# Kernel tuning notes

Hardware: AMD Instinct MI355X
Metric: run time of the kernel (lower is better)

The kernel has to match this reference:

```python
import jax, jax.numpy as jnp
import numpy as np
from jax import lax

N, D, H, E = 8192, 1024, 4096, 8


def setup_inputs() -> dict:
    key = jax.random.key(0)
    ks = jax.random.split(key, 7)
    s = 0.02
    return {
        "x": jax.random.normal(ks[0], (N, D), dtype=jnp.float32),
        "Wr": jax.random.normal(ks[1], (E, D), dtype=jnp.float32) * s,
        "br": jnp.zeros((E,), dtype=jnp.float32),
        "Wup": jax.random.normal(ks[2], (E, H, D), dtype=jnp.float32) * s,
        "bup": jnp.zeros((E, H), dtype=jnp.float32),
        "Wdown": jax.random.normal(ks[3], (E, D, H), dtype=jnp.float32) * s,
        "bdown": jnp.zeros((E, D), dtype=jnp.float32),
    }


def reference(x, Wr, br, Wup, bup, Wdown, bdown):
    # Router: softmax over logits; only argmax is used (softmax is monotone,
    # argmax of softmax == argmax of logits).
    logits = x @ Wr.T + br            # [N, E]
    scores = jax.nn.softmax(logits, axis=-1)
    top1 = jnp.argmax(scores, axis=-1)  # [N] int

    out0 = jnp.zeros_like(x)

    def body(out, ew):
        i, Wu, bu, Wd, bd = ew
        h = jax.nn.silu(x @ Wu.T + bu)   # [N, H]
        y = h @ Wd.T + bd                # [N, D]
        out = jnp.where((top1 == i)[:, None], y, out)
        return out, None

    idx = jnp.arange(Wup.shape[0])
    out, _ = lax.scan(body, out0, (idx, Wup, bup, Wdown, bdown))
    return out
```

## Files before the change

kernel.cpp:

```cpp
#include <hip/hip_runtime.h>

#define NT 8192
#define DD 1024
#define HH 4096
#define EE 8

typedef __attribute__((ext_vector_type(8))) short short8;
typedef __attribute__((ext_vector_type(4))) float f32x4;

__device__ __forceinline__ unsigned short f2bf(float f) {
    unsigned int u = __float_as_uint(f);
    u += 0x7FFFu + ((u >> 16) & 1u);
    return (unsigned short)(u >> 16);
}

__device__ __forceinline__ void gload_lds16(const void* g, void* l) {
    __builtin_amdgcn_global_load_lds(
        (const __attribute__((address_space(1))) unsigned int*)g,
        (__attribute__((address_space(3))) unsigned int*)l, 16, 0, 0);
}

__global__ __launch_bounds__(256) void cvt_kernel(const float* __restrict__ src,
                                                  unsigned short* __restrict__ dst) {
    size_t i = ((size_t)blockIdx.x * 256 + threadIdx.x) * 4;
    float4 v = *(const float4*)(src + i);
    ushort4 o;
    o.x = f2bf(v.x); o.y = f2bf(v.y); o.z = f2bf(v.z); o.w = f2bf(v.w);
    *(ushort4*)(dst + i) = o;
}

__global__ __launch_bounds__(256) void router_kernel(const float* __restrict__ x,
                                                     const float* __restrict__ Wr,
                                                     const float* __restrict__ br,
                                                     int* __restrict__ counts,
                                                     int* __restrict__ tlist) {
    __shared__ float sW[EE * DD];
    const int t = threadIdx.x;
    for (int i = t; i < EE * DD / 4; i += 256)
        ((float4*)sW)[i] = ((const float4*)Wr)[i];
    __syncthreads();
    const int lane = t & 63;
    const int wv = t >> 6;
    const int token = blockIdx.x * 4 + wv;
    const float* xr = x + (size_t)token * DD;
    float acc[EE];
#pragma unroll
    for (int e = 0; e < EE; e++) acc[e] = 0.f;
    for (int k = lane; k < DD; k += 64) {
        float xv = xr[k];
#pragma unroll
        for (int e = 0; e < EE; e++) acc[e] += xv * sW[e * DD + k];
    }
#pragma unroll
    for (int off = 32; off > 0; off >>= 1) {
#pragma unroll
        for (int e = 0; e < EE; e++) acc[e] += __shfl_xor(acc[e], off);
    }
    if (lane == 0) {
        int best = 0;
        float bv = acc[0] + br[0];
#pragma unroll
        for (int e = 1; e < EE; e++) {
            float v = acc[e] + br[e];
            if (v > bv) { bv = v; best = e; }
        }
        int pos = atomicAdd(&counts[best], 1);
        tlist[best * NT + pos] = token;
    }
}

__global__ void offsets_kernel(const int* __restrict__ counts, int* __restrict__ offsets) {
    if (threadIdx.x == 0) {
        int s = 0;
        for (int e = 0; e < EE; e++) { offsets[e] = s; s += counts[e]; }
    }
}

__global__ __launch_bounds__(256) void up_gemm(const unsigned short* __restrict__ xb,
                                               const unsigned short* __restrict__ Wub,
                                               const float* __restrict__ bup,
                                               const int* __restrict__ counts,
                                               const int* __restrict__ tlist,
                                               const int* __restrict__ offsets,
                                               unsigned short* __restrict__ hbuf) {
    const int e = blockIdx.z;
    const int cnt = counts[e];
    const int m0 = blockIdx.y * 128;
    if (m0 >= cnt) return;
    const int n0 = blockIdx.x * 128;
    const int t = threadIdx.x;

    __shared__ unsigned short sA[128 * 32];
    __shared__ unsigned short sB[128 * 32];

    const int r0 = t >> 2;
    const int kc = t & 3;
    const int* tl = tlist + e * NT;
    const int c1 = cnt - 1;
    int ra = m0 + r0;      if (ra > c1) ra = c1;
    int rb = m0 + 64 + r0; if (rb > c1) rb = c1;
    const unsigned short* gA0 = xb + (size_t)tl[ra] * DD + kc * 8;
    const unsigned short* gA1 = xb + (size_t)tl[rb] * DD + kc * 8;
    const unsigned short* gB0 = Wub + ((size_t)e * HH + n0 + r0) * DD + kc * 8;
    const unsigned short* gB1 = Wub + ((size_t)e * HH + n0 + 64 + r0) * DD + kc * 8;
    unsigned short* lA0 = sA + t * 8;
    unsigned short* lA1 = sA + (t + 256) * 8;
    unsigned short* lB0 = sB + t * 8;
    unsigned short* lB1 = sB + (t + 256) * 8;

    const int lane = t & 63;
    const int wm = ((t >> 6) & 1) * 64;
    const int wn = (t >> 7) * 64;
    const int mrow = lane & 15;
    const int kq = lane >> 4;

    f32x4 acc[4][4];
#pragma unroll
    for (int i = 0; i < 4; i++)
#pragma unroll
        for (int j = 0; j < 4; j++)
            acc[i][j] = (f32x4){0.f, 0.f, 0.f, 0.f};

    for (int kt = 0; kt < DD; kt += 32) {
        __syncthreads();
        gload_lds16(gA0 + kt, lA0);
        gload_lds16(gA1 + kt, lA1);
        gload_lds16(gB0 + kt, lB0);
        gload_lds16(gB1 + kt, lB1);
        __syncthreads();
        short8 a[4], b[4];
#pragma unroll
        for (int i = 0; i < 4; i++) {
            a[i] = *(const short8*)(sA + (wm + i * 16 + mrow) * 32 + kq * 8);
            b[i] = *(const short8*)(sB + (wn + i * 16 + mrow) * 32 + kq * 8);
        }
#pragma unroll
        for (int i = 0; i < 4; i++)
#pragma unroll
            for (int j = 0; j < 4; j++)
                acc[i][j] = __builtin_amdgcn_mfma_f32_16x16x32_bf16(a[i], b[j], acc[i][j], 0, 0, 0);
    }

    const int off_e = offsets[e];
    float bias[4];
#pragma unroll
    for (int j = 0; j < 4; j++) bias[j] = bup[e * HH + n0 + wn + j * 16 + mrow];
#pragma unroll
    for (int i = 0; i < 4; i++) {
#pragma unroll
        for (int r = 0; r < 4; r++) {
            int m = m0 + wm + i * 16 + kq * 4 + r;
            if (m < cnt) {
                unsigned short* hrow = hbuf + (size_t)(off_e + m) * HH + n0 + wn + mrow;
#pragma unroll
                for (int j = 0; j < 4; j++) {
                    float v = acc[i][j][r] + bias[j];
                    v = v / (1.f + __expf(-v));
                    hrow[j * 16] = f2bf(v);
                }
            }
        }
    }
}

__global__ __launch_bounds__(256) void down_gemm(const unsigned short* __restrict__ hbuf,
                                                 const unsigned short* __restrict__ Wdb,
                                                 const float* __restrict__ bdown,
                                                 const int* __restrict__ counts,
                                                 const int* __restrict__ tlist,
                                                 const int* __restrict__ offsets,
                                                 float* __restrict__ out) {
    const int e = blockIdx.z;
    const int cnt = counts[e];
    const int m0 = blockIdx.y * 128;
    if (m0 >= cnt) return;
    const int n0 = blockIdx.x * 128;
    const int t = threadIdx.x;

    __shared__ unsigned short sA[128 * 32];
    __shared__ unsigned short sB[128 * 32];

    const int r0 = t >> 2;
    const int kc = t & 3;
    const int off_e = offsets[e];
    const int c1 = cnt - 1;
    int ra = m0 + r0;      if (ra > c1) ra = c1;
    int rb = m0 + 64 + r0; if (rb > c1) rb = c1;
    const unsigned short* gA0 = hbuf + (size_t)(off_e + ra) * HH + kc * 8;
    const unsigned short* gA1 = hbuf + (size_t)(off_e + rb) * HH + kc * 8;
    const unsigned short* gB0 = Wdb + ((size_t)e * DD + n0 + r0) * HH + kc * 8;
    const unsigned short* gB1 = Wdb + ((size_t)e * DD + n0 + 64 + r0) * HH + kc * 8;
    unsigned short* lA0 = sA + t * 8;
    unsigned short* lA1 = sA + (t + 256) * 8;
    unsigned short* lB0 = sB + t * 8;
    unsigned short* lB1 = sB + (t + 256) * 8;

    const int lane = t & 63;
    const int wm = ((t >> 6) & 1) * 64;
    const int wn = (t >> 7) * 64;
    const int mrow = lane & 15;
    const int kq = lane >> 4;

    f32x4 acc[4][4];
#pragma unroll
    for (int i = 0; i < 4; i++)
#pragma unroll
        for (int j = 0; j < 4; j++)
            acc[i][j] = (f32x4){0.f, 0.f, 0.f, 0.f};

    for (int kt = 0; kt < HH; kt += 32) {
        __syncthreads();
        gload_lds16(gA0 + kt, lA0);
        gload_lds16(gA1 + kt, lA1);
        gload_lds16(gB0 + kt, lB0);
        gload_lds16(gB1 + kt, lB1);
        __syncthreads();
        short8 a[4], b[4];
#pragma unroll
        for (int i = 0; i < 4; i++) {
            a[i] = *(const short8*)(sA + (wm + i * 16 + mrow) * 32 + kq * 8);
            b[i] = *(const short8*)(sB + (wn + i * 16 + mrow) * 32 + kq * 8);
        }
#pragma unroll
        for (int i = 0; i < 4; i++)
#pragma unroll
            for (int j = 0; j < 4; j++)
                acc[i][j] = __builtin_amdgcn_mfma_f32_16x16x32_bf16(a[i], b[j], acc[i][j], 0, 0, 0);
    }

    const int* tl = tlist + e * NT;
    float bias[4];
#pragma unroll
    for (int j = 0; j < 4; j++) bias[j] = bdown[e * DD + n0 + wn + j * 16 + mrow];
#pragma unroll
    for (int i = 0; i < 4; i++) {
#pragma unroll
        for (int r = 0; r < 4; r++) {
            int m = m0 + wm + i * 16 + kq * 4 + r;
            if (m < cnt) {
                int token = tl[m];
                float* orow = out + (size_t)token * DD + n0 + wn + mrow;
#pragma unroll
                for (int j = 0; j < 4; j++)
                    orow[j * 16] = acc[i][j][r] + bias[j];
            }
        }
    }
}

extern "C" void kernel_launch(void* const* d_in, const int* in_sizes, int n_in,
                              void* d_out, int out_size, void* d_ws, size_t ws_size,
                              hipStream_t stream) {
    const float* x     = (const float*)d_in[0];
    const float* Wr    = (const float*)d_in[1];
    const float* br    = (const float*)d_in[2];
    const float* Wup   = (const float*)d_in[3];
    const float* bup   = (const float*)d_in[4];
    const float* Wdown = (const float*)d_in[5];
    const float* bdown = (const float*)d_in[6];
    float* out = (float*)d_out;

    char* w = (char*)d_ws;
    int* counts  = (int*)w;               w += 256;
    int* offsets = (int*)w;               w += 256;
    int* tlist   = (int*)w;               w += (size_t)EE * NT * 4;
    unsigned short* xb   = (unsigned short*)w;  w += (size_t)NT * DD * 2;
    unsigned short* hbuf = (unsigned short*)w;  w += (size_t)NT * HH * 2;
    unsigned short* Wub  = (unsigned short*)w;  w += (size_t)EE * HH * DD * 2;
    unsigned short* Wdb  = (unsigned short*)w;

    hipMemsetAsync(counts, 0, EE * sizeof(int), stream);

    cvt_kernel<<<(NT * DD) / 1024, 256, 0, stream>>>(x, xb);
    cvt_kernel<<<((size_t)EE * HH * DD) / 1024, 256, 0, stream>>>(Wup, Wub);
    cvt_kernel<<<((size_t)EE * DD * HH) / 1024, 256, 0, stream>>>(Wdown, Wdb);
    router_kernel<<<NT / 4, 256, 0, stream>>>(x, Wr, br, counts, tlist);
    offsets_kernel<<<1, 64, 0, stream>>>(counts, offsets);

    dim3 gu(HH / 128, NT / 128, EE);
    up_gemm<<<gu, 256, 0, stream>>>(xb, Wub, bup, counts, tlist, offsets, hbuf);
    dim3 gd(DD / 128, NT / 128, EE);
    down_gemm<<<gd, 256, 0, stream>>>(hbuf, Wdb, bdown, counts, tlist, offsets, out);
}
```

Before: 673.5 us.

## Split-K down GEMM with atomics, pre-gather tokens, merge weight conversions

Splits the down-projection's K dimension in two. The grid doubles to fill more CUs, and results are accumulated into a zeroed output with float atomicAdd. A new gather kernel converts and packs the routed tokens contiguously per expert, so the up GEMM reads dense rows instead of indirect ones. The two weight conversions are merged into one launch. The changes add an output memset and atomic write traffic, and the split makes summation order nondeterministic.

```diff
diff --git a/kernel.cpp b/kernel.cpp
--- a/kernel.cpp
+++ b/kernel.cpp
@@ -20,13 +20,19 @@
         (__attribute__((address_space(3))) unsigned int*)l, 16, 0, 0);
 }
 
-__global__ __launch_bounds__(256) void cvt_kernel(const float* __restrict__ src,
-                                                  unsigned short* __restrict__ dst) {
+__global__ __launch_bounds__(256) void cvtw_kernel(const float* __restrict__ a,
+                                                   const float* __restrict__ b,
+                                                   unsigned short* __restrict__ da,
+                                                   unsigned short* __restrict__ db) {
+    const size_t half = (size_t)EE * HH * DD;
     size_t i = ((size_t)blockIdx.x * 256 + threadIdx.x) * 4;
-    float4 v = *(const float4*)(src + i);
+    const float* s; unsigned short* d;
+    if (i < half) { s = a + i; d = da + i; }
+    else          { s = b + (i - half); d = db + (i - half); }
+    float4 v = *(const float4*)s;
     ushort4 o;
     o.x = f2bf(v.x); o.y = f2bf(v.y); o.z = f2bf(v.z); o.w = f2bf(v.w);
-    *(ushort4*)(dst + i) = o;
+    *(ushort4*)d = o;
 }
 
 __global__ __launch_bounds__(256) void router_kernel(const float* __restrict__ x,
@@ -76,11 +82,32 @@
     }
 }
 
-__global__ __launch_bounds__(256) void up_gemm(const unsigned short* __restrict__ xb,
+__global__ __launch_bounds__(256) void gather_kernel(const float* __restrict__ x,
+                                                     const int* __restrict__ tlist,
+                                                     const int* __restrict__ offsets,
+                                                     unsigned short* __restrict__ xg) {
+    const int row = blockIdx.x * 4 + (threadIdx.x >> 6);
+    const int lane = threadIdx.x & 63;
+    int e = 0;
+#pragma unroll
+    for (int k = 1; k < EE; k++)
+        if (row >= offsets[k]) e = k;
+    const int token = tlist[e * NT + row - offsets[e]];
+    const float4* src = (const float4*)(x + (size_t)token * DD);
+    ushort4* dst = (ushort4*)(xg + (size_t)row * DD);
+#pragma unroll
+    for (int it = 0; it < 4; it++) {
+        float4 v = src[it * 64 + lane];
+        ushort4 o;
+        o.x = f2bf(v.x); o.y = f2bf(v.y); o.z = f2bf(v.z); o.w = f2bf(v.w);
+        dst[it * 64 + lane] = o;
+    }
+}
+
+__global__ __launch_bounds__(256) void up_gemm(const unsigned short* __restrict__ xg,
                                                const unsigned short* __restrict__ Wub,
                                                const float* __restrict__ bup,
                                                const int* __restrict__ counts,
-                                               const int* __restrict__ tlist,
                                                const int* __restrict__ offsets,
                                                unsigned short* __restrict__ hbuf) {
     const int e = blockIdx.z;
@@ -89,18 +116,18 @@
     if (m0 >= cnt) return;
     const int n0 = blockIdx.x * 128;
     const int t = threadIdx.x;
+    const int off_e = offsets[e];
 
     __shared__ unsigned short sA[128 * 32];
     __shared__ unsigned short sB[128 * 32];
 
     const int r0 = t >> 2;
     const int kc = t & 3;
-    const int* tl = tlist + e * NT;
     const int c1 = cnt - 1;
     int ra = m0 + r0;      if (ra > c1) ra = c1;
     int rb = m0 + 64 + r0; if (rb > c1) rb = c1;
-    const unsigned short* gA0 = xb + (size_t)tl[ra] * DD + kc * 8;
-    const unsigned short* gA1 = xb + (size_t)tl[rb] * DD + kc * 8;
+    const unsigned short* gA0 = xg + (size_t)(off_e + ra) * DD + kc * 8;
+    const unsigned short* gA1 = xg + (size_t)(off_e + rb) * DD + kc * 8;
     const unsigned short* gB0 = Wub + ((size_t)e * HH + n0 + r0) * DD + kc * 8;
     const unsigned short* gB1 = Wub + ((size_t)e * HH + n0 + 64 + r0) * DD + kc * 8;
     unsigned short* lA0 = sA + t * 8;
@@ -141,7 +168,6 @@
                 acc[i][j] = __builtin_amdgcn_mfma_f32_16x16x32_bf16(a[i], b[j], acc[i][j], 0, 0, 0);
     }
 
-    const int off_e = offsets[e];
     float bias[4];
 #pragma unroll
     for (int j = 0; j < 4; j++) bias[j] = bup[e * HH + n0 + wn + j * 16 + mrow];
@@ -170,7 +196,8 @@
                                                  const int* __restrict__ tlist,
                                                  const int* __restrict__ offsets,
                                                  float* __restrict__ out) {
-    const int e = blockIdx.z;
+    const int e = blockIdx.z >> 1;
+    const int s = blockIdx.z & 1;
     const int cnt = counts[e];
     const int m0 = blockIdx.y * 128;
     if (m0 >= cnt) return;
@@ -208,7 +235,9 @@
         for (int j = 0; j < 4; j++)
             acc[i][j] = (f32x4){0.f, 0.f, 0.f, 0.f};
 
-    for (int kt = 0; kt < HH; kt += 32) {
+    const int kbeg = s * (HH / 2);
+    const int kend = kbeg + (HH / 2);
+    for (int kt = kbeg; kt < kend; kt += 32) {
         __syncthreads();
         gload_lds16(gA0 + kt, lA0);
         gload_lds16(gA1 + kt, lA1);
@@ -231,7 +260,8 @@
     const int* tl = tlist + e * NT;
     float bias[4];
 #pragma unroll
-    for (int j = 0; j < 4; j++) bias[j] = bdown[e * DD + n0 + wn + j * 16 + mrow];
+    for (int j = 0; j < 4; j++)
+        bias[j] = (s == 0) ? bdown[e * DD + n0 + wn + j * 16 + mrow] : 0.f;
 #pragma unroll
     for (int i = 0; i < 4; i++) {
 #pragma unroll
@@ -242,7 +272,7 @@
                 float* orow = out + (size_t)token * DD + n0 + wn + mrow;
 #pragma unroll
                 for (int j = 0; j < 4; j++)
-                    orow[j * 16] = acc[i][j][r] + bias[j];
+                    atomicAdd(&orow[j * 16], acc[i][j][r] + bias[j]);
             }
         }
     }
@@ -264,21 +294,21 @@
     int* counts  = (int*)w;               w += 256;
     int* offsets = (int*)w;               w += 256;
     int* tlist   = (int*)w;               w += (size_t)EE * NT * 4;
-    unsigned short* xb   = (unsigned short*)w;  w += (size_t)NT * DD * 2;
+    unsigned short* xg   = (unsigned short*)w;  w += (size_t)NT * DD * 2;
     unsigned short* hbuf = (unsigned short*)w;  w += (size_t)NT * HH * 2;
     unsigned short* Wub  = (unsigned short*)w;  w += (size_t)EE * HH * DD * 2;
     unsigned short* Wdb  = (unsigned short*)w;
 
     hipMemsetAsync(counts, 0, EE * sizeof(int), stream);
-
-    cvt_kernel<<<(NT * DD) / 1024, 256, 0, stream>>>(x, xb);
-    cvt_kernel<<<((size_t)EE * HH * DD) / 1024, 256, 0, stream>>>(Wup, Wub);
-    cvt_kernel<<<((size_t)EE * DD * HH) / 1024, 256, 0, stream>>>(Wdown, Wdb);
+    hipMemsetAsync(out, 0, (size_t)NT * DD * sizeof(float), stream);
+
+    cvtw_kernel<<<(2 * (size_t)EE * HH * DD) / 1024, 256, 0, stream>>>(Wup, Wdown, Wub, Wdb);
     router_kernel<<<NT / 4, 256, 0, stream>>>(x, Wr, br, counts, tlist);
     offsets_kernel<<<1, 64, 0, stream>>>(counts, offsets);
+    gather_kernel<<<NT / 4, 256, 0, stream>>>(x, tlist, offsets, xg);
 
     dim3 gu(HH / 128, NT / 128, EE);
-    up_gemm<<<gu, 256, 0, stream>>>(xb, Wub, bup, counts, tlist, offsets, hbuf);
-    dim3 gd(DD / 128, NT / 128, EE);
+    up_gemm<<<gu, 256, 0, stream>>>(xg, Wub, bup, counts, offsets, hbuf);
+    dim3 gd(DD / 128, NT / 128, EE * 2);
     down_gemm<<<gd, 256, 0, stream>>>(hbuf, Wdb, bdown, counts, tlist, offsets, out);
 }
```

After: 699.8 us. 3.9% more time.
